# Optimization experiments

Measured on AMD Instinct MI355X. Metric: run time of the kernel, lower is better.

## Reference

```python
import jax, jax.numpy as jnp
import numpy as np

R = 3           # disp_range = (3, 3)
DU = 2 * R + 1  # 7 displacements per axis, 49 total
PNAMES = ['mn_w1','mn_b1','mn_w2','mn_b2','mn_w3','mn_b3','mn_w4','mn_b4','mn_wd','mn_bd','mn_w5','mn_b5','dap_w','dap_b','me_w1','me_b1','me_w2','me_b2','me_w3','me_b3','gz1_w','gz1_b','gr1_w','gr1_b','gq1_w','gq1_b','gz2_w','gz2_b','gr2_w','gr2_b','gq2_w','gq2_b','fh_w1','fh_b1','fh_w2','fh_b2']


def conv2d(x, w, b, stride=(1, 1), padding=((1, 1), (1, 1))):
    y = jax.lax.conv_general_dilated(x, w, stride, padding, dimension_numbers=('NCHW', 'OIHW', 'NCHW'))
    return y + b[None, :, None, None]


def warp_backwards(f, flow):
    # bilinear backward warp with zero padding; flow[:,0]=u (x offset), flow[:,1]=v (y offset)
    B, C, H, W = f.shape
    gy, gx = jnp.meshgrid(jnp.arange(H, dtype=flow.dtype), jnp.arange(W, dtype=flow.dtype), indexing='ij')
    x = gx[None] + flow[:, 0]
    y = gy[None] + flow[:, 1]
    x0, y0 = jnp.floor(x), jnp.floor(y)
    wx, wy = x - x0, y - y0

    def corner(yy, xx, wgt):
        valid = (yy >= 0) & (yy <= H - 1) & (xx >= 0) & (xx <= W - 1)
        yc = jnp.clip(yy, 0, H - 1).astype(jnp.int32)
        xc = jnp.clip(xx, 0, W - 1).astype(jnp.int32)
        g = jax.vmap(lambda fb, yb, xb: fb[:, yb, xb])(f, yc, xc)  # (B,C,H,W)
        return g * (wgt * valid.astype(f.dtype))[:, None]

    return (corner(y0, x0, (1 - wy) * (1 - wx)) + corner(y0, x0 + 1, (1 - wy) * wx)
            + corner(y0 + 1, x0, wy * (1 - wx)) + corner(y0 + 1, x0 + 1, wy * wx))


def gru_step(h, x, wz, bz, wr, br, wq, bq, pad):
    hx = jnp.concatenate([h, x], axis=1)
    z = jax.nn.sigmoid(conv2d(hx, wz, bz, padding=pad))
    r = jax.nn.sigmoid(conv2d(hx, wr, br, padding=pad))
    q = jnp.tanh(conv2d(jnp.concatenate([r * h, x], axis=1), wq, bq, padding=pad))
    return (1.0 - z) * h + z * q


def _run(fmap1, fmap2, h, flow, P):
    B, C, H, W = fmap1.shape
    lrelu, relu = jax.nn.leaky_relu, jax.nn.relu
    # backward warp of fmap2 by current (detached) flow
    f2w = warp_backwards(fmap2, jax.lax.stop_gradient(flow))
    # --- correlation volume: 49 zero-padded shifts of warped fmap2, paired with fmap1 ---
    pad2 = jnp.pad(f2w, ((0, 0), (0, 0), (R, R), (R, R)))
    # k = i*DU + j  <->  shift (di, dj) = (i-R, j-R); shifted[...,y,x] = f2w[y+dj, x+di]
    shifted = jnp.stack([pad2[:, :, j:j + H, i:i + W] for i in range(DU) for j in range(DU)], axis=1)  # (B,49,C,H,W)
    valid = (jnp.sum(shifted, axis=2, keepdims=True) != 0).astype(fmap1.dtype)
    mvol = jnp.concatenate([jnp.broadcast_to(fmap1[:, None], shifted.shape), shifted], axis=2) * valid  # (B,49,2C,H,W)
    # --- matching net, applied per displacement ---
    x = mvol.reshape(B * DU * DU, 2 * C, H, W)
    x = relu(conv2d(x, P['mn_w1'], P['mn_b1']))
    x = relu(conv2d(x, P['mn_w2'], P['mn_b2'], stride=(2, 2)))
    x = relu(conv2d(x, P['mn_w3'], P['mn_b3']))
    x = relu(conv2d(x, P['mn_w4'], P['mn_b4']))
    # ConvTranspose2d(k=4, s=2, p=1) == lhs-dilated conv with pad 2
    x = jax.lax.conv_general_dilated(x, P['mn_wd'], (1, 1), ((2, 2), (2, 2)), lhs_dilation=(2, 2), dimension_numbers=('NCHW', 'OIHW', 'NCHW')) + P['mn_bd'][None, :, None, None]
    x = relu(x)
    x = conv2d(x, P['mn_w5'], P['mn_b5'])  # (B*49, 1, H, W)
    cvol = x.reshape(B, DU * DU, H, W)
    # --- displacement-aware projection: 1x1 conv across the 49 displacement channels ---
    cvol = jnp.einsum('ok,bkhw->bohw', P['dap_w'], cvol) + P['dap_b'][None, :, None, None]
    # --- motion encoder ---
    m = jnp.concatenate([cvol, fmap1, flow], axis=1)  # (B, 49+C+2, H, W)
    m = lrelu(conv2d(m, P['me_w1'], P['me_b1']))
    m = lrelu(conv2d(m, P['me_w2'], P['me_b2']))
    m = conv2d(m, P['me_w3'], P['me_b3'])             # (B, 94, H, W)
    xg = jnp.concatenate([m, flow], axis=1)           # (B, 96, H, W)
    # --- separable conv GRU: horizontal (1x5) then vertical (5x1) pass ---
    h = gru_step(h, xg, P['gz1_w'], P['gz1_b'], P['gr1_w'], P['gr1_b'], P['gq1_w'], P['gq1_b'], ((0, 0), (2, 2)))
    h = gru_step(h, xg, P['gz2_w'], P['gz2_b'], P['gr2_w'], P['gr2_b'], P['gq2_w'], P['gq2_b'], ((2, 2), (0, 0)))
    # --- flow head: softmax over 49 displacements, expectation of displacement grid ---
    s = lrelu(jnp.einsum('oi,bihw->bohw', P['fh_w1'], h) + P['fh_b1'][None, :, None, None])
    s = lrelu(jnp.einsum('oi,bihw->bohw', P['fh_w2'], s) + P['fh_b2'][None, :, None, None])
    prob = jax.nn.softmax(s, axis=1)  # (B, 49, H, W)
    dr = jnp.arange(-R, R + 1, dtype=fmap1.dtype)
    disp = jnp.stack([jnp.broadcast_to(dr[:, None], (DU, DU)), jnp.broadcast_to(dr[None, :], (DU, DU))], axis=0).reshape(2, DU * DU)
    d = jnp.einsum('bkhw,ck->bchw', prob, disp)
    return h, flow + d


def _params(key):
    shapes = {'mn_w1': (96, 64, 3, 3), 'mn_b1': (96,), 'mn_w2': (128, 96, 3, 3), 'mn_b2': (128,), 'mn_w3': (128, 128, 3, 3), 'mn_b3': (128,), 'mn_w4': (64, 128, 3, 3), 'mn_b4': (64,), 'mn_wd': (32, 64, 4, 4), 'mn_bd': (32,), 'mn_w5': (1, 32, 3, 3), 'mn_b5': (1,), 'dap_w': (49, 49), 'dap_b': (49,), 'me_w1': (128, 83, 3, 3), 'me_b1': (128,), 'me_w2': (128, 128, 3, 3), 'me_b2': (128,), 'me_w3': (94, 128, 3, 3), 'me_b3': (94,), 'gz1_w': (128, 224, 1, 5), 'gz1_b': (128,), 'gr1_w': (128, 224, 1, 5), 'gr1_b': (128,), 'gq1_w': (128, 224, 1, 5), 'gq1_b': (128,), 'gz2_w': (128, 224, 5, 1), 'gz2_b': (128,), 'gr2_w': (128, 224, 5, 1), 'gr2_b': (128,), 'gq2_w': (128, 224, 5, 1), 'gq2_b': (128,), 'fh_w1': (256, 128), 'fh_b1': (256,), 'fh_w2': (49, 256), 'fh_b2': (49,)}
    keys = jax.random.split(key, len(shapes))
    return {n: jax.random.normal(k, s, dtype=jnp.float32) * 0.05 for (n, s), k in zip(shapes.items(), keys)}


def setup_inputs():
    key = jax.random.key(0)
    k1, k2, k3, k4, kp = jax.random.split(key, 5)
    B, C, H, W, HID = 2, 32, 64, 96, 128
    inp = {'fmap1': jax.random.normal(k1, (B, C, H, W), jnp.float32),
           'fmap2': jax.random.normal(k2, (B, C, H, W), jnp.float32),
           'h': jax.random.normal(k3, (B, HID, H, W), jnp.float32),
           'flow': jax.random.normal(k4, (B, 2, H, W), jnp.float32),
           'i': 0}
    inp.update(_params(kp))
    return inp


def reference(fmap1, fmap2, h, flow, mn_w1, mn_b1, mn_w2, mn_b2, mn_w3, mn_b3, mn_w4, mn_b4, mn_wd, mn_bd, mn_w5, mn_b5, dap_w, dap_b, me_w1, me_b1, me_w2, me_b2, me_w3, me_b3, gz1_w, gz1_b, gr1_w, gr1_b, gq1_w, gq1_b, gz2_w, gz2_b, gr2_w, gr2_b, gq2_w, gq2_b, fh_w1, fh_b1, fh_w2, fh_b2, i):
    ps = (mn_w1, mn_b1, mn_w2, mn_b2, mn_w3, mn_b3, mn_w4, mn_b4, mn_wd, mn_bd, mn_w5, mn_b5, dap_w, dap_b, me_w1, me_b1, me_w2, me_b2, me_w3, me_b3, gz1_w, gz1_b, gr1_w, gr1_b, gq1_w, gq1_b, gz2_w, gz2_b, gr2_w, gr2_b, gq2_w, gq2_b, fh_w1, fh_b1, fh_w2, fh_b2)
    return _run(fmap1, fmap2, h, flow, dict(zip(PNAMES, ps)))
```

## Files before the change

kernel.cpp:

```cpp
#include <hip/hip_runtime.h>
#include <math.h>

typedef unsigned short u16;
typedef unsigned int u32;
typedef __attribute__((ext_vector_type(8))) short bf16x8;
typedef __attribute__((ext_vector_type(4))) float f32x4;

#define HWW 6144

__device__ __forceinline__ float sigmoidf_(float x) { return 1.f / (1.f + expf(-x)); }
__device__ __forceinline__ float lrelu_(float x) { return x >= 0.f ? x : 0.01f * x; }
__device__ __forceinline__ u16 f2bf(float f) {
    u32 u = __float_as_uint(f);
    u += 0x7fffu + ((u >> 16) & 1u);
    return (u16)(u >> 16);
}
__device__ __forceinline__ float bf2f(u16 h) { return __uint_as_float(((u32)h) << 16); }
__device__ __forceinline__ u32 pk2(float a, float b) { return (u32)f2bf(a) | ((u32)f2bf(b) << 16); }

__device__ __forceinline__ void gload_lds16(const u16* g, u16* l) {
    __builtin_amdgcn_global_load_lds((const __attribute__((address_space(1))) void*)g,
                                     (__attribute__((address_space(3))) void*)l, 16, 0, 0);
}

struct WJob { const float* src; unsigned long dstOff; int OC, rowOff, IC, ICP, NT; unsigned long cum; };
struct WJobs { WJob j[16]; long total; };

__global__ __launch_bounds__(256) void k_wt_all(WJobs J, u16* __restrict__ base)
{
    long i = (long)blockIdx.x * 256 + threadIdx.x;
    if (i >= J.total) return;
    int jb = 0;
    #pragma unroll
    for (int k = 1; k < 16; ++k) if (i >= (long)J.j[k].cum) jb = k;
    WJob w = J.j[jb];
    long local = i - (long)w.cum;
    int c = (int)(local % w.ICP);
    int t = (int)((local / w.ICP) % w.NT);
    int o = (int)(local / ((long)w.ICP * w.NT));
    float val = (c < w.IC) ? w.src[((long)o * w.IC + c) * w.NT + t] : 0.f;
    base[w.dstOff + ((long)(w.rowOff + o) * w.NT + t) * w.ICP + c] = f2bf(val);
}

__global__ __launch_bounds__(256) void k_wt_dq(const float* __restrict__ w, u16* __restrict__ dst)
{
    int i = blockIdx.x * 256 + threadIdx.x;
    if (i >= 32768) return;
    int c = i & 63; int t = (i >> 6) & 3; int o = (i >> 8) & 31; int q = i >> 13;
    int ry = q >> 1, rx = q & 1, ta = t >> 1, tb = t & 1;
    int ky = ry + 2 * ta, kx = rx + 2 * tb;
    float val = w[(((long)o * 64 + c) * 4 + ky) * 4 + kx];
    dst[(long)q * 8192 + o * 256 + t * 64 + c] = f2bf(val);
}

__global__ __launch_bounds__(256) void k_wt5(const float* __restrict__ w, float* __restrict__ wt)
{
    int i = blockIdx.x * 256 + threadIdx.x;
    if (i >= 288) return;
    int t = i % 9, c = i / 9;
    wt[t * 32 + c] = w[c * 9 + t];
}

__global__ void k_catb(const float* __restrict__ a, const float* __restrict__ b, float* __restrict__ d)
{
    int i = threadIdx.x;
    if (i < 128) d[i] = a[i];
    else if (i < 256) d[i] = b[i - 128];
}

__global__ __launch_bounds__(256) void k_prep_f1(const float* __restrict__ fmap1, u16* __restrict__ f1bf)
{
    int gid = blockIdx.x * 256 + threadIdx.x;
    if (gid >= 24576) return;
    int idx = gid >> 1, half = gid & 1;
    int b = idx / HWW, p = idx % HWW;
    const float* fb = fmap1 + (long)b * 32 * HWW + p + (long)(half * 16) * HWW;
    u32 pk[8];
    #pragma unroll
    for (int c2 = 0; c2 < 8; ++c2)
        pk[c2] = pk2(fb[(long)(2 * c2) * HWW], fb[(long)(2 * c2 + 1) * HWW]);
    u16* op = f1bf + ((long)idx << 5) + half * 16;
    ((uint4*)op)[0] = make_uint4(pk[0], pk[1], pk[2], pk[3]);
    ((uint4*)op)[1] = make_uint4(pk[4], pk[5], pk[6], pk[7]);
}

__global__ __launch_bounds__(256) void k_warp(const float* __restrict__ fmap2, const float* __restrict__ flow,
                                              u16* __restrict__ f2wbf, float* __restrict__ cs)
{
    int gid = blockIdx.x * 256 + threadIdx.x;
    if (gid >= 24576) return;
    int idx = gid >> 1, half = gid & 1;
    int b = idx / HWW, p = idx % HWW, y = p / 96, x = p % 96;
    float u = flow[(b * 2 + 0) * HWW + p], v = flow[(b * 2 + 1) * HWW + p];
    float fx = (float)x + u, fy = (float)y + v;
    float fx0 = floorf(fx), fy0 = floorf(fy);
    float wx = fx - fx0, wy = fy - fy0;
    int x0 = (int)fx0, y0i = (int)fy0, x1 = x0 + 1, y1 = y0i + 1;
    bool vx0 = x0 >= 0 && x0 < 96, vx1 = x1 >= 0 && x1 < 96;
    bool vy0 = y0i >= 0 && y0i < 64, vy1 = y1 >= 0 && y1 < 64;
    float m00 = (vy0 && vx0) ? (1.f - wy) * (1.f - wx) : 0.f;
    float m01 = (vy0 && vx1) ? (1.f - wy) * wx : 0.f;
    float m10 = (vy1 && vx0) ? wy * (1.f - wx) : 0.f;
    float m11 = (vy1 && vx1) ? wy * wx : 0.f;
    int cx0 = min(max(x0, 0), 95), cx1 = min(max(x1, 0), 95);
    int cy0 = min(max(y0i, 0), 63), cy1 = min(max(y1, 0), 63);
    int i00 = cy0 * 96 + cx0, i01 = cy0 * 96 + cx1, i10 = cy1 * 96 + cx0, i11 = cy1 * 96 + cx1;
    const float* fb = fmap2 + (long)b * 32 * HWW + (long)(half * 16) * HWW;
    float s = 0.f; u32 pk[8];
    #pragma unroll
    for (int c2 = 0; c2 < 8; ++c2) {
        const float* fa = fb + (long)(2 * c2) * HWW;
        const float* fc = fb + (long)(2 * c2 + 1) * HWW;
        float g0 = m00 * fa[i00] + m01 * fa[i01] + m10 * fa[i10] + m11 * fa[i11];
        float g1 = m00 * fc[i00] + m01 * fc[i01] + m10 * fc[i10] + m11 * fc[i11];
        s += g0 + g1;
        pk[c2] = pk2(g0, g1);
    }
    u16* op = f2wbf + ((long)idx << 5) + half * 16;
    ((uint4*)op)[0] = make_uint4(pk[0], pk[1], pk[2], pk[3]);
    ((uint4*)op)[1] = make_uint4(pk[4], pk[5], pk[6], pk[7]);
    float stot = s + __shfl_xor(s, 1);
    if (half == 0) cs[idx] = stot;
}

template<int BM, int BN, int MODE, int KH, int KW, int PH, int PW, int STRIDE, int ACT, int OUTF32,
         int IH, int IW, int OH, int OW, int ICP, int NKT>
__global__ __launch_bounds__(256) void k_gemm(
    const u16* __restrict__ A0, const u16* __restrict__ A1,
    const float* __restrict__ csm, const u16* __restrict__ Wb,
    const float* __restrict__ bias, const u16* __restrict__ zpg,
    u16* __restrict__ outb, u16* __restrict__ outb2, float* __restrict__ outf,
    int OC, int ldc, int coff, int nOff)
{
    constexpr int WAVES_M = (BM == 64) ? 2 : ((BN == 128) ? 2 : 4);
    constexpr int WAVES_N = 4 / WAVES_M;
    constexpr int WTM = BM / WAVES_M;
    constexpr int WTN = BN / WAVES_N;
    constexpr int MF = WTM / 16;
    constexpr int NF = WTN / 16;
    __shared__ u16 As[2][BM * 32];
    __shared__ u16 Bs[2][BN * 32];
    int tid = threadIdx.x, lane = tid & 63, wid = tid >> 6;
    constexpr int AIW = BM / 64;
    constexpr int BI  = BN / 16;
    constexpr int BIW = (BI >= 4) ? (BI / 4) : 1;
    int ryz = 0, rxz = 0;
    if (MODE == 2) { ryz = blockIdx.z >> 1; rxz = blockIdx.z & 1; }
    const u16* WbZ = Wb + (MODE == 2 ? (long)blockIdx.z * 32 * 256 : 0);
    int n0 = blockIdx.y * BN;
    int chunk = lane & 3, sub = lane >> 2;

    const u16* aB0[AIW]; const u16* aB1[AIW]; u32 am[AIW];
    #pragma unroll
    for (int j = 0; j < AIW; ++j) {
        int row = wid * (BM / 4) + j * 16 + sub;
        int gm = blockIdx.x * BM + row;
        constexpr int OHW = (MODE == 1) ? 6144 : ((MODE == 2) ? 1536 : OH * OW);
        constexpr int OWW = (MODE == 1) ? 96 : ((MODE == 2) ? 48 : OW);
        int nI = gm / OHW, rem = gm - nI * OHW;
        int y0 = rem / OWW, x0 = rem - y0 * OWW;
        aB1[j] = A0; am[j] = 0;
        if (MODE == 0) {
            aB0[j] = A0 + ((long)nI * IH * IW + (long)y0 * STRIDE * IW + (long)x0 * STRIDE) * ICP + chunk * 8;
            u32 m = 0;
            #pragma unroll
            for (int t = 0; t < KH * KW; ++t) {
                int dy = t / KW - PH, dx = t % KW - PW;
                int iy = y0 * STRIDE + dy, ix = x0 * STRIDE + dx;
                m |= ((iy >= 0 && iy < IH && ix >= 0 && ix < IW) ? 1u : 0u) << t;
            }
            am[j] = m;
        } else if (MODE == 1) {
            int n = nOff + nI, bI = n / 49, kd = n - bI * 49;
            int di = kd / 7 - 3, dj = kd % 7 - 3;
            long bH = (long)bI * 6144;
            aB0[j] = A0 + ((bH + rem) << 5) + chunk * 8;
            aB1[j] = A1 + ((bH + (y0 + dj) * 96 + (x0 + di)) << 5) + chunk * 8;
            u32 m = 0;
            #pragma unroll
            for (int t = 0; t < 9; ++t) {
                int dy = t / 3 - 1, dx = t % 3 - 1;
                int yy = y0 + dy, xx = x0 + dx, ys = yy + dj, xs = xx + di;
                bool v = yy >= 0 && yy < 64 && xx >= 0 && xx < 96 && ys >= 0 && ys < 64 && xs >= 0 && xs < 96;
                if (v) v = (csm[bI * 6144 + ys * 96 + xs] != 0.f);
                m |= (v ? 1u : 0u) << t;
            }
            am[j] = m;
        } else {
            int iy0 = y0 + ryz - 1, ix0 = x0 + rxz - 1;
            aB0[j] = A0 + ((long)nI * 1536 + (long)iy0 * 48 + ix0) * 64 + chunk * 8;
            u32 m = 0;
            #pragma unroll
            for (int t = 0; t < 4; ++t) {
                int ta = t >> 1, tb = t & 1;
                int iy = iy0 + ta, ix = ix0 + tb;
                m |= ((iy >= 0 && iy < 32 && ix >= 0 && ix < 48) ? 1u : 0u) << t;
            }
            am[j] = m;
        }
    }
    const u16* bB[BIW];
    bool doB = (BI >= 4) || (wid < BI);
    #pragma unroll
    for (int j = 0; j < BIW; ++j) {
        int rowB = ((BI >= 4) ? wid * (BN / 4) + j * 16 : wid * 16) + sub;
        bB[j] = WbZ + (long)(n0 + rowB) * (NKT * 32) + chunk * 8;
    }

    auto stage = [&](int kt, int bn) {
        #pragma unroll
        for (int j = 0; j < AIW; ++j) {
            const u16* g;
            if (MODE == 0) {
                constexpr int KTC = ICP / 32;
                int t = kt / KTC, c0 = (kt - t * KTC) << 5;
                int dy = t / KW - PH, dx = t % KW - PW;
                bool v = (am[j] >> t) & 1u;
                g = v ? aB0[j] + (long)(dy * IW + dx) * ICP + c0 : zpg;
            } else if (MODE == 1) {
                int t = kt >> 1, half = kt & 1;
                int dy = t / 3 - 1, dx = t % 3 - 1;
                bool v = (am[j] >> t) & 1u;
                const u16* b = half ? aB1[j] : aB0[j];
                g = v ? b + ((dy * 96 + dx) << 5) : zpg;
            } else {
                int t = kt >> 1, c0 = (kt & 1) << 5;
                int ta = t >> 1, tb = t & 1;
                bool v = (am[j] >> t) & 1u;
                g = v ? aB0[j] + (ta * 48 + tb) * 64 + c0 : zpg;
            }
            gload_lds16(g, &As[bn][(wid * (BM / 4) + j * 16) * 32]);
        }
        if (doB) {
            #pragma unroll
            for (int j = 0; j < BIW; ++j) {
                int base = (BI >= 4) ? wid * (BN / 4) + j * 16 : wid * 16;
                gload_lds16(bB[j] + kt * 32, &Bs[bn][base * 32]);
            }
        }
    };

    int wm = (WAVES_N == 2) ? (wid >> 1) : wid;
    int wn = (WAVES_N == 2) ? (wid & 1) : 0;
    int fr = lane & 15, fg = lane >> 4;
    f32x4 acc[MF][NF];
    #pragma unroll
    for (int i = 0; i < MF; ++i)
        #pragma unroll
        for (int j = 0; j < NF; ++j)
            acc[i][j] = (f32x4){0.f, 0.f, 0.f, 0.f};

    stage(0, 0);
    __syncthreads();

    #pragma unroll
    for (int kt = 0; kt < NKT; ++kt) {
        int cur = kt & 1;
        if (kt + 1 < NKT) stage(kt + 1, cur ^ 1);
        bf16x8 af[MF], bv[NF];
        #pragma unroll
        for (int i = 0; i < MF; ++i)
            af[i] = *(const bf16x8*)&As[cur][(wm * WTM + i * 16 + fr) * 32 + fg * 8];
        #pragma unroll
        for (int j = 0; j < NF; ++j)
            bv[j] = *(const bf16x8*)&Bs[cur][(wn * WTN + j * 16 + fr) * 32 + fg * 8];
        #pragma unroll
        for (int i = 0; i < MF; ++i)
            #pragma unroll
            for (int j = 0; j < NF; ++j)
                acc[i][j] = __builtin_amdgcn_mfma_f32_16x16x32_bf16(af[i], bv[j], acc[i][j], 0, 0, 0);
        if (kt + 1 < NKT) __syncthreads();
    }

    #pragma unroll
    for (int i = 0; i < MF; ++i) {
        #pragma unroll
        for (int j = 0; j < NF; ++j) {
            int nn = n0 + wn * WTN + j * 16 + fr;
            if (nn >= OC) continue;
            #pragma unroll
            for (int rr = 0; rr < 4; ++rr) {
                int mloc = wm * WTM + i * 16 + fg * 4 + rr;
                long gm = (long)blockIdx.x * BM + mloc;
                float v = acc[i][j][rr] + bias[nn];
                if (ACT == 1) v = fmaxf(v, 0.f);
                else if (ACT == 2) v = lrelu_(v);
                if (OUTF32) {
                    outf[gm * ldc + coff + nn] = v;
                } else if (MODE == 2) {
                    int nI = (int)(gm / 1536); int rq = (int)(gm - (long)nI * 1536);
                    int Y = rq / 48, X = rq - (rq / 48) * 48;
                    long di = (((long)nI * 64 + 2 * Y + ryz) * 96 + (2 * X + rxz)) * 32 + nn;
                    outb[di] = f2bf(v);
                } else {
                    long di = gm * ldc + coff + nn;
                    u16 hv = f2bf(v);
                    outb[di] = hv;
                    if (outb2) outb2[di] = hv;
                }
            }
        }
    }
}

__global__ __launch_bounds__(256) void k_conv5n(const u16* __restrict__ x5, const float* __restrict__ w5t,
                                                const float* __restrict__ b5, u16* __restrict__ cvolT,
                                                int N, int n0)
{
    int idx = blockIdx.x * 256 + threadIdx.x;
    if (idx >= N * HWW) return;
    int nl = idx / HWW, p = idx % HWW, y = p / 96, x = p % 96;
    float acc = b5[0];
    #pragma unroll
    for (int t = 0; t < 9; ++t) {
        int iy = y + t / 3 - 1, ix = x + t % 3 - 1;
        if (iy < 0 || iy >= 64 || ix < 0 || ix >= 96) continue;
        const u16* sp = x5 + (((long)nl * HWW + iy * 96 + ix) << 5);
        const float* wt_ = w5t + t * 32;
        #pragma unroll
        for (int c8 = 0; c8 < 4; ++c8) {
            uint4 v = *(const uint4*)(sp + c8 * 8);
            acc = fmaf(bf2f((u16)(v.x & 0xffffu)), wt_[c8 * 8 + 0], acc);
            acc = fmaf(bf2f((u16)(v.x >> 16)),     wt_[c8 * 8 + 1], acc);
            acc = fmaf(bf2f((u16)(v.y & 0xffffu)), wt_[c8 * 8 + 2], acc);
            acc = fmaf(bf2f((u16)(v.y >> 16)),     wt_[c8 * 8 + 3], acc);
            acc = fmaf(bf2f((u16)(v.z & 0xffffu)), wt_[c8 * 8 + 4], acc);
            acc = fmaf(bf2f((u16)(v.z >> 16)),     wt_[c8 * 8 + 5], acc);
            acc = fmaf(bf2f((u16)(v.w & 0xffffu)), wt_[c8 * 8 + 6], acc);
            acc = fmaf(bf2f((u16)(v.w >> 16)),     wt_[c8 * 8 + 7], acc);
        }
    }
    int n = n0 + nl;
    int b = n / 49, k = n - b * 49;
    cvolT[((long)b * HWW + p) * 64 + k] = f2bf(acc);
}

__global__ __launch_bounds__(256) void k_me_tail(const float* __restrict__ fmap1, const float* __restrict__ flow,
                                                 u16* __restrict__ mein)
{
    int gid = blockIdx.x * 256 + threadIdx.x;
    if (gid >= 73728) return;
    int j = gid / 12288, idx = gid - j * 12288;
    int b = idx / HWW, p = idx % HWW;
    int c0 = 49 + j * 8;
    u16* mp = mein + (long)idx * 96;
    #pragma unroll
    for (int q = 0; q < 8; ++q) {
        int c = c0 + q;
        if (c >= 96) break;
        float v;
        if (c < 81) v = fmap1[((long)(b * 32 + (c - 49))) * HWW + p];
        else if (c == 81) v = flow[(b * 2 + 0) * HWW + p];
        else if (c == 82) v = flow[(b * 2 + 1) * HWW + p];
        else v = 0.f;
        mp[c] = f2bf(v);
    }
}

__global__ __launch_bounds__(256) void k_set_head(const float* __restrict__ h, const float* __restrict__ flow,
                                                  float* __restrict__ hst, u16* __restrict__ hx,
                                                  u16* __restrict__ hx2)
{
    int gid = blockIdx.x * 256 + threadIdx.x;
    if (gid >= 49152) return;
    int cq = gid / 12288, idx = gid - cq * 12288;
    int b = idx / HWW, p = idx % HWW;
    int c0 = cq * 32;
    const float* hp = h + (long)b * 128 * HWW + p;
    float* hs = hst + (long)idx * 128;
    u16* hxp = hx + (long)idx * 224;
    #pragma unroll
    for (int c = c0; c < c0 + 32; c += 8) {
        float v[8];
        #pragma unroll
        for (int q = 0; q < 8; ++q) v[q] = hp[(long)(c + q) * HWW];
        *(float4*)&hs[c] = make_float4(v[0], v[1], v[2], v[3]);
        *(float4*)&hs[c + 4] = make_float4(v[4], v[5], v[6], v[7]);
        uint4 pk = make_uint4(pk2(v[0], v[1]), pk2(v[2], v[3]), pk2(v[4], v[5]), pk2(v[6], v[7]));
        *(uint4*)&hxp[c] = pk;
    }
    if (cq == 0) {
        u16 uu = f2bf(flow[(b * 2 + 0) * HWW + p]);
        u16 vv = f2bf(flow[(b * 2 + 1) * HWW + p]);
        long o = (long)idx * 224;
        hx[o + 222] = uu; hx[o + 223] = vv;
        hx2[o + 222] = uu; hx2[o + 223] = vv;
    }
}

__global__ __launch_bounds__(256) void k_post_zr(const float* __restrict__ azr, const float* __restrict__ hst,
                                                 float* __restrict__ z, u16* __restrict__ hx2)
{
    int gid = blockIdx.x * 256 + threadIdx.x;
    if (gid >= 49152) return;
    int cq = gid / 12288, idx = gid - cq * 12288;
    int c0 = cq * 32;
    const float* ap = azr + (long)idx * 256;
    const float* hs = hst + (long)idx * 128;
    float* zp = z + (long)idx * 128;
    u16* xp = hx2 + (long)idx * 224;
    #pragma unroll
    for (int c = c0; c < c0 + 32; c += 8) {
        float4 a0 = *(const float4*)&ap[c], a1 = *(const float4*)&ap[c + 4];
        float4 r0 = *(const float4*)&ap[128 + c], r1 = *(const float4*)&ap[128 + c + 4];
        float4 h0 = *(const float4*)&hs[c], h1v = *(const float4*)&hs[c + 4];
        float z0 = sigmoidf_(a0.x), z1 = sigmoidf_(a0.y), z2 = sigmoidf_(a0.z), z3 = sigmoidf_(a0.w);
        float z4 = sigmoidf_(a1.x), z5 = sigmoidf_(a1.y), z6 = sigmoidf_(a1.z), z7 = sigmoidf_(a1.w);
        *(float4*)&zp[c] = make_float4(z0, z1, z2, z3);
        *(float4*)&zp[c + 4] = make_float4(z4, z5, z6, z7);
        float rh0 = sigmoidf_(r0.x) * h0.x, rh1 = sigmoidf_(r0.y) * h0.y;
        float rh2 = sigmoidf_(r0.z) * h0.z, rh3 = sigmoidf_(r0.w) * h0.w;
        float rh4 = sigmoidf_(r1.x) * h1v.x, rh5 = sigmoidf_(r1.y) * h1v.y;
        float rh6 = sigmoidf_(r1.z) * h1v.z, rh7 = sigmoidf_(r1.w) * h1v.w;
        uint4 pk = make_uint4(pk2(rh0, rh1), pk2(rh2, rh3), pk2(rh4, rh5), pk2(rh6, rh7));
        *(uint4*)&xp[c] = pk;
    }
}

template<int FIN>
__global__ __launch_bounds__(256) void k_post_q(const float* __restrict__ aq, const float* __restrict__ z,
                                                const float* __restrict__ hst, float* __restrict__ h1f,
                                                u16* __restrict__ hxdst, float* __restrict__ outH)
{
    int gid = blockIdx.x * 256 + threadIdx.x;
    if (gid >= 49152) return;
    int cq = gid / 12288, idx = gid - cq * 12288;
    int b = idx / HWW, p = idx % HWW;
    int c0 = cq * 32;
    const float* ap = aq + (long)idx * 128;
    const float* zp = z + (long)idx * 128;
    const float* hs = hst + (long)idx * 128;
    #pragma unroll
    for (int c = c0; c < c0 + 32; c += 8) {
        float hn[8];
        #pragma unroll
        for (int q = 0; q < 8; ++q) {
            float qq = tanhf(ap[c + q]);
            float zv = zp[c + q];
            hn[q] = (1.f - zv) * hs[c + q] + zv * qq;
        }
        uint4 pk = make_uint4(pk2(hn[0], hn[1]), pk2(hn[2], hn[3]), pk2(hn[4], hn[5]), pk2(hn[6], hn[7]));
        if (FIN == 0) {
            *(float4*)&h1f[(long)idx * 128 + c] = make_float4(hn[0], hn[1], hn[2], hn[3]);
            *(float4*)&h1f[(long)idx * 128 + c + 4] = make_float4(hn[4], hn[5], hn[6], hn[7]);
            *(uint4*)&hxdst[(long)idx * 224 + c] = pk;
        } else {
            #pragma unroll
            for (int q = 0; q < 8; ++q)
                outH[((long)(b * 128 + c + q)) * HWW + p] = hn[q];
            *(uint4*)&hxdst[(long)idx * 128 + c] = pk;
        }
    }
}

__global__ __launch_bounds__(256) void k_soft(const float* __restrict__ s2, const float* __restrict__ flow,
                                              float* __restrict__ outFlow)
{
    int idx = blockIdx.x * 256 + threadIdx.x;
    if (idx >= 12288) return;
    int b = idx / HWW, p = idx % HWW;
    const float* sp = s2 + (long)idx * 64;
    float lg[49];
    #pragma unroll
    for (int k = 0; k < 48; k += 4) {
        float4 v = *(const float4*)&sp[k];
        lg[k] = v.x; lg[k + 1] = v.y; lg[k + 2] = v.z; lg[k + 3] = v.w;
    }
    lg[48] = sp[48];
    float m = -1e30f;
    #pragma unroll
    for (int k = 0; k < 49; ++k) m = fmaxf(m, lg[k]);
    float s = 0.f, a0 = 0.f, a1 = 0.f;
    #pragma unroll
    for (int k = 0; k < 49; ++k) {
        float e = expf(lg[k] - m);
        s += e;
        a0 += e * (float)(k / 7 - 3);
        a1 += e * (float)(k % 7 - 3);
    }
    float inv = 1.f / s;
    outFlow[(long)(b * 2 + 0) * HWW + p] = flow[(long)(b * 2 + 0) * HWW + p] + a0 * inv;
    outFlow[(long)(b * 2 + 1) * HWW + p] = flow[(long)(b * 2 + 1) * HWW + p] + a1 * inv;
}

extern "C" void kernel_launch(void* const* d_in, const int* in_sizes, int n_in,
                              void* d_out, int out_size, void* d_ws, size_t ws_size,
                              hipStream_t stream)
{
    const float* fmap1 = (const float*)d_in[0];
    const float* fmap2 = (const float*)d_in[1];
    const float* h     = (const float*)d_in[2];
    const float* flow  = (const float*)d_in[3];
    int pb = (in_sizes[4] == 1) ? 5 : 4;
    const float* mn_w1 = (const float*)d_in[pb + 0];
    const float* mn_b1 = (const float*)d_in[pb + 1];
    const float* mn_w2 = (const float*)d_in[pb + 2];
    const float* mn_b2 = (const float*)d_in[pb + 3];
    const float* mn_w3 = (const float*)d_in[pb + 4];
    const float* mn_b3 = (const float*)d_in[pb + 5];
    const float* mn_w4 = (const float*)d_in[pb + 6];
    const float* mn_b4 = (const float*)d_in[pb + 7];
    const float* mn_wd = (const float*)d_in[pb + 8];
    const float* mn_bd = (const float*)d_in[pb + 9];
    const float* mn_w5 = (const float*)d_in[pb + 10];
    const float* mn_b5 = (const float*)d_in[pb + 11];
    const float* dap_w = (const float*)d_in[pb + 12];
    const float* dap_b = (const float*)d_in[pb + 13];
    const float* me_w1 = (const float*)d_in[pb + 14];
    const float* me_b1 = (const float*)d_in[pb + 15];
    const float* me_w2 = (const float*)d_in[pb + 16];
    const float* me_b2 = (const float*)d_in[pb + 17];
    const float* me_w3 = (const float*)d_in[pb + 18];
    const float* me_b3 = (const float*)d_in[pb + 19];
    const float* gz1_w = (const float*)d_in[pb + 20];
    const float* gz1_b = (const float*)d_in[pb + 21];
    const float* gr1_w = (const float*)d_in[pb + 22];
    const float* gr1_b = (const float*)d_in[pb + 23];
    const float* gq1_w = (const float*)d_in[pb + 24];
    const float* gq1_b = (const float*)d_in[pb + 25];
    const float* gz2_w = (const float*)d_in[pb + 26];
    const float* gz2_b = (const float*)d_in[pb + 27];
    const float* gr2_w = (const float*)d_in[pb + 28];
    const float* gr2_b = (const float*)d_in[pb + 29];
    const float* gq2_w = (const float*)d_in[pb + 30];
    const float* gq2_b = (const float*)d_in[pb + 31];
    const float* fh_w1 = (const float*)d_in[pb + 32];
    const float* fh_b1 = (const float*)d_in[pb + 33];
    const float* fh_w2 = (const float*)d_in[pb + 34];
    const float* fh_b2 = (const float*)d_in[pb + 35];

    char* wsB = (char*)d_ws;
    size_t off = 0;
    auto alc = [&](size_t bytes) { size_t o = off; off = (off + bytes + 255) & ~(size_t)255; return o; };

    size_t o_zpg  = alc(256);
    size_t o_wc1  = alc(128 * 576 * 2);
    size_t o_wc2  = alc(128 * 864 * 2);
    size_t o_wc3  = alc((size_t)128 * 1152 * 2);
    size_t o_wc4  = alc((size_t)64 * 1152 * 2);
    size_t o_wdq  = alc(32768 * 2);
    size_t o_wme1 = alc(128 * 864 * 2);
    size_t o_wme2 = alc((size_t)128 * 1152 * 2);
    size_t o_wme3 = alc((size_t)128 * 1152 * 2);
    size_t o_wzr1 = alc((size_t)256 * 1120 * 2);
    size_t o_wq1  = alc((size_t)128 * 1120 * 2);
    size_t o_wzr2 = alc((size_t)256 * 1120 * 2);
    size_t o_wq2  = alc((size_t)128 * 1120 * 2);
    size_t o_wfh1 = alc(256 * 128 * 2);
    size_t o_wfh2 = alc(64 * 256 * 2);
    size_t o_wdapb= alc(64 * 64 * 2);
    size_t o_w5t  = alc(288 * 4);
    size_t o_bzr1 = alc(256 * 4);
    size_t o_bzr2 = alc(256 * 4);
    size_t wArenaBytes = off;

    size_t o_f1bf = alc((size_t)12288 * 32 * 2);
    size_t o_f2wb = alc((size_t)12288 * 32 * 2);
    size_t o_cs   = alc(12288 * 4);
    size_t o_cvolT= alc((size_t)12288 * 64 * 2);

    const int CH = 49;
    size_t sharedBase = off;
    size_t offA = sharedBase;
    auto alcA = [&](size_t bytes) { size_t o = offA; offA = (offA + bytes + 255) & ~(size_t)255; return o; };
    size_t o_x1 = alcA((size_t)CH * 6144 * 96 * 2);
    size_t o_x2 = alcA((size_t)98 * 1536 * 128 * 2);
    size_t o_x3 = alcA((size_t)98 * 1536 * 128 * 2);
    size_t o_x4 = alcA((size_t)98 * 1536 * 64 * 2);
    size_t o_x5 = alcA((size_t)98 * 6144 * 32 * 2);
    size_t offB2 = sharedBase;
    auto alcB = [&](size_t bytes) { size_t o = offB2; offB2 = (offB2 + bytes + 255) & ~(size_t)255; return o; };
    size_t o_mein = alcB((size_t)12288 * 96 * 2);
    size_t o_m1   = alcB((size_t)12288 * 128 * 2);
    size_t o_m2   = alcB((size_t)12288 * 128 * 2);
    size_t o_hx   = alcB((size_t)12288 * 224 * 2);
    size_t o_hx2  = alcB((size_t)12288 * 224 * 2);
    size_t o_h2bf = alcB((size_t)12288 * 128 * 2);
    size_t o_s1b  = alcB((size_t)12288 * 256 * 2);
    size_t o_hst  = alcB((size_t)12288 * 128 * 4);
    size_t o_h1f  = alcB((size_t)12288 * 128 * 4);
    size_t o_zf   = alcB((size_t)12288 * 128 * 4);
    size_t o_azr  = alcB((size_t)12288 * 256 * 4);
    size_t o_aqf  = alcB((size_t)12288 * 128 * 4);
    size_t o_s2   = alcB((size_t)12288 * 64 * 4);

    u16* wbase = (u16*)wsB;
    u16* zpg  = (u16*)(wsB + o_zpg);
    u16* wdq  = (u16*)(wsB + o_wdq);
    float* w5t = (float*)(wsB + o_w5t);
    float* bzr1 = (float*)(wsB + o_bzr1);
    float* bzr2 = (float*)(wsB + o_bzr2);
    u16* wc1  = (u16*)(wsB + o_wc1);   u16* wc2  = (u16*)(wsB + o_wc2);
    u16* wc3  = (u16*)(wsB + o_wc3);   u16* wc4  = (u16*)(wsB + o_wc4);
    u16* wme1 = (u16*)(wsB + o_wme1);  u16* wme2 = (u16*)(wsB + o_wme2);
    u16* wme3 = (u16*)(wsB + o_wme3);
    u16* wzr1 = (u16*)(wsB + o_wzr1);  u16* wq1  = (u16*)(wsB + o_wq1);
    u16* wzr2 = (u16*)(wsB + o_wzr2);  u16* wq2  = (u16*)(wsB + o_wq2);
    u16* wfh1 = (u16*)(wsB + o_wfh1);  u16* wfh2 = (u16*)(wsB + o_wfh2);
    u16* wdapb= (u16*)(wsB + o_wdapb);

    u16* f1bf = (u16*)(wsB + o_f1bf);  u16* f2wb = (u16*)(wsB + o_f2wb);
    float* cs = (float*)(wsB + o_cs);
    u16* cvolT = (u16*)(wsB + o_cvolT);
    u16* x1 = (u16*)(wsB + o_x1); u16* x2 = (u16*)(wsB + o_x2); u16* x3 = (u16*)(wsB + o_x3);
    u16* x4 = (u16*)(wsB + o_x4); u16* x5 = (u16*)(wsB + o_x5);
    u16* mein = (u16*)(wsB + o_mein);
    u16* m1 = (u16*)(wsB + o_m1); u16* m2 = (u16*)(wsB + o_m2);
    u16* hx = (u16*)(wsB + o_hx); u16* hx2 = (u16*)(wsB + o_hx2);
    u16* h2bf = (u16*)(wsB + o_h2bf);  u16* s1b = (u16*)(wsB + o_s1b);
    float* hst = (float*)(wsB + o_hst); float* h1f = (float*)(wsB + o_h1f);
    float* zf = (float*)(wsB + o_zf); float* azr = (float*)(wsB + o_azr);
    float* aqf = (float*)(wsB + o_aqf); float* s2 = (float*)(wsB + o_s2);

    float* outH = (float*)d_out;
    float* outFlow = outH + (long)2 * 128 * HWW;

    auto nb = [](long total, int bs) { return (unsigned)((total + bs - 1) / bs); };

    hipMemsetAsync(wsB, 0, wArenaBytes, stream);
    hipMemsetAsync(wsB + o_cvolT, 0, (size_t)12288 * 64 * 2, stream);

    WJobs J;
    {
        auto mk = [](const float* src, size_t dstOffBytes, int OC, int rowOff, int IC, int ICP, int NT) {
            WJob w; w.src = src; w.dstOff = dstOffBytes / 2; w.OC = OC; w.rowOff = rowOff;
            w.IC = IC; w.ICP = ICP; w.NT = NT; w.cum = 0; return w;
        };
        J.j[0]  = mk(mn_w1, o_wc1, 96, 0, 64, 64, 9);
        J.j[1]  = mk(mn_w2, o_wc2, 128, 0, 96, 96, 9);
        J.j[2]  = mk(mn_w3, o_wc3, 128, 0, 128, 128, 9);
        J.j[3]  = mk(mn_w4, o_wc4, 64, 0, 128, 128, 9);
        J.j[4]  = mk(me_w1, o_wme1, 128, 0, 83, 96, 9);
        J.j[5]  = mk(me_w2, o_wme2, 128, 0, 128, 128, 9);
        J.j[6]  = mk(me_w3, o_wme3, 94, 0, 128, 128, 9);
        J.j[7]  = mk(gz1_w, o_wzr1, 128, 0, 224, 224, 5);
        J.j[8]  = mk(gr1_w, o_wzr1, 128, 128, 224, 224, 5);
        J.j[9]  = mk(gq1_w, o_wq1, 128, 0, 224, 224, 5);
        J.j[10] = mk(gz2_w, o_wzr2, 128, 0, 224, 224, 5);
        J.j[11] = mk(gr2_w, o_wzr2, 128, 128, 224, 224, 5);
        J.j[12] = mk(gq2_w, o_wq2, 128, 0, 224, 224, 5);
        J.j[13] = mk(fh_w1, o_wfh1, 256, 0, 128, 128, 1);
        J.j[14] = mk(fh_w2, o_wfh2, 49, 0, 256, 256, 1);
        J.j[15] = mk(dap_w, o_wdapb, 49, 0, 49, 64, 1);
        long cum = 0;
        for (int k = 0; k < 16; ++k) {
            J.j[k].cum = cum;
            cum += (long)J.j[k].OC * J.j[k].NT * J.j[k].ICP;
        }
        J.total = cum;
    }
    k_wt_all<<<nb(J.total, 256), 256, 0, stream>>>(J, wbase);
    k_wt_dq<<<nb(32768, 256), 256, 0, stream>>>(mn_wd, wdq);
    k_wt5<<<2, 256, 0, stream>>>(mn_w5, w5t);
    k_catb<<<1, 256, 0, stream>>>(gz1_b, gr1_b, bzr1);
    k_catb<<<1, 256, 0, stream>>>(gz2_b, gr2_b, bzr2);

    k_prep_f1<<<nb(24576, 256), 256, 0, stream>>>(fmap1, f1bf);
    k_warp<<<nb(24576, 256), 256, 0, stream>>>(fmap2, flow, f2wb, cs);

    for (int n0 = 0; n0 < 98; n0 += CH) {
        k_gemm<128,128,1,3,3,1,1,1,1,0,64,96,64,96,32,18><<<dim3(2352, 1), 256, 0, stream>>>(
            f1bf, f2wb, cs, wc1, mn_b1, zpg, x1, nullptr, nullptr, 96, 96, 0, n0);
        k_gemm<128,128,0,3,3,1,1,2,1,0,64,96,32,48,96,27><<<dim3(588, 1), 256, 0, stream>>>(
            x1, nullptr, nullptr, wc2, mn_b2, zpg, x2 + (long)n0 * 196608, nullptr, nullptr, 128, 128, 0, 0);
    }
    k_gemm<128,128,0,3,3,1,1,1,1,0,32,48,32,48,128,36><<<dim3(1176, 1), 256, 0, stream>>>(
        x2, nullptr, nullptr, wc3, mn_b3, zpg, x3, nullptr, nullptr, 128, 128, 0, 0);
    k_gemm<128,64,0,3,3,1,1,1,1,0,32,48,32,48,128,36><<<dim3(1176, 1), 256, 0, stream>>>(
        x3, nullptr, nullptr, wc4, mn_b4, zpg, x4, nullptr, nullptr, 64, 64, 0, 0);
    k_gemm<128,32,2,4,4,2,2,1,1,0,32,48,32,48,64,8><<<dim3(1176, 1, 4), 256, 0, stream>>>(
        x4, nullptr, nullptr, wdq, mn_bd, zpg, x5, nullptr, nullptr, 32, 32, 0, 0);
    k_conv5n<<<nb(98L * HWW, 256), 256, 0, stream>>>(x5, w5t, mn_b5, cvolT, 98, 0);

    k_gemm<64,64,0,1,1,0,0,1,0,0,64,96,64,96,64,2><<<dim3(192, 1), 256, 0, stream>>>(
        cvolT, nullptr, nullptr, wdapb, dap_b, zpg, mein, nullptr, nullptr, 49, 96, 0, 0);
    k_me_tail<<<nb(73728, 256), 256, 0, stream>>>(fmap1, flow, mein);

    k_gemm<64,128,0,3,3,1,1,1,2,0,64,96,64,96,96,27><<<dim3(192, 1), 256, 0, stream>>>(
        mein, nullptr, nullptr, wme1, me_b1, zpg, m1, nullptr, nullptr, 128, 128, 0, 0);
    k_gemm<64,128,0,3,3,1,1,1,2,0,64,96,64,96,128,36><<<dim3(192, 1), 256, 0, stream>>>(
        m1, nullptr, nullptr, wme2, me_b2, zpg, m2, nullptr, nullptr, 128, 128, 0, 0);
    k_gemm<64,128,0,3,3,1,1,1,0,0,64,96,64,96,128,36><<<dim3(192, 1), 256, 0, stream>>>(
        m2, nullptr, nullptr, wme3, me_b3, zpg, hx, hx2, nullptr, 94, 224, 128, 0);

    k_set_head<<<nb(49152, 256), 256, 0, stream>>>(h, flow, hst, hx, hx2);
    k_gemm<64,128,0,1,5,0,2,1,0,1,64,96,64,96,224,35><<<dim3(192, 2), 256, 0, stream>>>(
        hx, nullptr, nullptr, wzr1, bzr1, zpg, nullptr, nullptr, azr, 256, 256, 0, 0);
    k_post_zr<<<nb(49152, 256), 256, 0, stream>>>(azr, hst, zf, hx2);
    k_gemm<64,128,0,1,5,0,2,1,0,1,64,96,64,96,224,35><<<dim3(192, 1), 256, 0, stream>>>(
        hx2, nullptr, nullptr, wq1, gq1_b, zpg, nullptr, nullptr, aqf, 128, 128, 0, 0);
    k_post_q<0><<<nb(49152, 256), 256, 0, stream>>>(aqf, zf, hst, h1f, hx, nullptr);

    k_gemm<64,128,0,5,1,2,0,1,0,1,64,96,64,96,224,35><<<dim3(192, 2), 256, 0, stream>>>(
        hx, nullptr, nullptr, wzr2, bzr2, zpg, nullptr, nullptr, azr, 256, 256, 0, 0);
    k_post_zr<<<nb(49152, 256), 256, 0, stream>>>(azr, h1f, zf, hx2);
    k_gemm<64,128,0,5,1,2,0,1,0,1,64,96,64,96,224,35><<<dim3(192, 1), 256, 0, stream>>>(
        hx2, nullptr, nullptr, wq2, gq2_b, zpg, nullptr, nullptr, aqf, 128, 128, 0, 0);
    k_post_q<1><<<nb(49152, 256), 256, 0, stream>>>(aqf, zf, h1f, nullptr, h2bf, outH);

    k_gemm<64,128,0,1,1,0,0,1,2,0,64,96,64,96,128,4><<<dim3(192, 2), 256, 0, stream>>>(
        h2bf, nullptr, nullptr, wfh1, fh_b1, zpg, s1b, nullptr, nullptr, 256, 256, 0, 0);
    k_gemm<64,64,0,1,1,0,0,1,2,1,64,96,64,96,256,8><<<dim3(192, 1), 256, 0, stream>>>(
        s1b, nullptr, nullptr, wfh2, fh_b2, zpg, nullptr, nullptr, s2, 49, 64, 0, 0);
    k_soft<<<nb(12288, 256), 256, 0, stream>>>(s2, flow, outFlow);
}
```

Baseline: 730.8 us.

## Fuse GRU gate epilogues into GEMMs and trim N-tile to 96

Moves the GRU z/r sigmoid, r*h product and q tanh/state-update epilogues into the conv GEMM output stage, so the separate post kernels and the fp32 azr/aqf intermediate buffers are gone. It also generalises the wave split and B-tile loading so BN=96 tiles work, and uses them for the first correlation conv and me3, where OC is 96 or 94, to avoid computing padded columns. The fused epilogue uses scattered scalar stores and adds extra memory reads per output element, which may be less coalesced than the dedicated vectorised kernels.

```diff
diff --git a/kernel.cpp b/kernel.cpp
--- a/kernel.cpp
+++ b/kernel.cpp
@@ -132,8 +132,8 @@
     u16* __restrict__ outb, u16* __restrict__ outb2, float* __restrict__ outf,
     int OC, int ldc, int coff, int nOff)
 {
-    constexpr int WAVES_M = (BM == 64) ? 2 : ((BN == 128) ? 2 : 4);
-    constexpr int WAVES_N = 4 / WAVES_M;
+    constexpr int WAVES_N = (BN >= 128) ? 2 : 1;
+    constexpr int WAVES_M = 4 / WAVES_N;
     constexpr int WTM = BM / WAVES_M;
     constexpr int WTN = BN / WAVES_N;
     constexpr int MF = WTM / 16;
@@ -142,8 +142,8 @@
     __shared__ u16 Bs[2][BN * 32];
     int tid = threadIdx.x, lane = tid & 63, wid = tid >> 6;
     constexpr int AIW = BM / 64;
-    constexpr int BI  = BN / 16;
-    constexpr int BIW = (BI >= 4) ? (BI / 4) : 1;
+    constexpr int BG  = BN / 16;
+    constexpr int BJW = (BG + 3) / 4;
     int ryz = 0, rxz = 0;
     if (MODE == 2) { ryz = blockIdx.z >> 1; rxz = blockIdx.z & 1; }
     const u16* WbZ = Wb + (MODE == 2 ? (long)blockIdx.z * 32 * 256 : 0);
@@ -199,12 +199,12 @@
             am[j] = m;
         }
     }
-    const u16* bB[BIW];
-    bool doB = (BI >= 4) || (wid < BI);
-    #pragma unroll
-    for (int j = 0; j < BIW; ++j) {
-        int rowB = ((BI >= 4) ? wid * (BN / 4) + j * 16 : wid * 16) + sub;
-        bB[j] = WbZ + (long)(n0 + rowB) * (NKT * 32) + chunk * 8;
+    const u16* bB[BJW];
+    #pragma unroll
+    for (int j = 0; j < BJW; ++j) {
+        int g = wid + 4 * j;
+        int gc = (g < BG) ? g : 0;
+        bB[j] = WbZ + (long)(n0 + gc * 16 + sub) * (NKT * 32) + chunk * 8;
     }
 
     auto stage = [&](int kt, int bn) {
@@ -231,12 +231,10 @@
             }
             gload_lds16(g, &As[bn][(wid * (BM / 4) + j * 16) * 32]);
         }
-        if (doB) {
-            #pragma unroll
-            for (int j = 0; j < BIW; ++j) {
-                int base = (BI >= 4) ? wid * (BN / 4) + j * 16 : wid * 16;
-                gload_lds16(bB[j] + kt * 32, &Bs[bn][base * 32]);
-            }
+        #pragma unroll
+        for (int j = 0; j < BJW; ++j) {
+            int g = wid + 4 * j;
+            if (g < BG) gload_lds16(bB[j] + kt * 32, &Bs[bn][g * 512]);
         }
     };
 
@@ -285,8 +283,23 @@
                 float v = acc[i][j][rr] + bias[nn];
                 if (ACT == 1) v = fmaxf(v, 0.f);
                 else if (ACT == 2) v = lrelu_(v);
-                if (OUTF32) {
+                if (OUTF32 == 1) {
                     outf[gm * ldc + coff + nn] = v;
+                } else if (OUTF32 == 2) {
+                    float s = sigmoidf_(v);
+                    if (nn < 128) outf[gm * 128 + nn] = s;
+                    else outb[gm * 224 + (nn - 128)] = f2bf(s * csm[gm * 128 + (nn - 128)]);
+                } else if (OUTF32 == 3 || OUTF32 == 4) {
+                    float zv = ((const float*)A1)[gm * 128 + nn];
+                    float hnew = (1.f - zv) * csm[gm * 128 + nn] + zv * tanhf(v);
+                    if (OUTF32 == 3) {
+                        outf[gm * 128 + nn] = hnew;
+                        outb[gm * 224 + nn] = f2bf(hnew);
+                    } else {
+                        int bb = (int)(gm / 6144), pp = (int)(gm - (long)bb * 6144);
+                        outf[((long)(bb * 128 + nn)) * 6144 + pp] = hnew;
+                        outb[gm * 128 + nn] = f2bf(hnew);
+                    }
                 } else if (MODE == 2) {
                     int nI = (int)(gm / 1536); int rq = (int)(gm - (long)nI * 1536);
                     int Y = rq / 48, X = rq - (rq / 48) * 48;
@@ -385,71 +398,6 @@
         long o = (long)idx * 224;
         hx[o + 222] = uu; hx[o + 223] = vv;
         hx2[o + 222] = uu; hx2[o + 223] = vv;
-    }
-}
-
-__global__ __launch_bounds__(256) void k_post_zr(const float* __restrict__ azr, const float* __restrict__ hst,
-                                                 float* __restrict__ z, u16* __restrict__ hx2)
-{
-    int gid = blockIdx.x * 256 + threadIdx.x;
-    if (gid >= 49152) return;
-    int cq = gid / 12288, idx = gid - cq * 12288;
-    int c0 = cq * 32;
-    const float* ap = azr + (long)idx * 256;
-    const float* hs = hst + (long)idx * 128;
-    float* zp = z + (long)idx * 128;
-    u16* xp = hx2 + (long)idx * 224;
-    #pragma unroll
-    for (int c = c0; c < c0 + 32; c += 8) {
-        float4 a0 = *(const float4*)&ap[c], a1 = *(const float4*)&ap[c + 4];
-        float4 r0 = *(const float4*)&ap[128 + c], r1 = *(const float4*)&ap[128 + c + 4];
-        float4 h0 = *(const float4*)&hs[c], h1v = *(const float4*)&hs[c + 4];
-        float z0 = sigmoidf_(a0.x), z1 = sigmoidf_(a0.y), z2 = sigmoidf_(a0.z), z3 = sigmoidf_(a0.w);
-        float z4 = sigmoidf_(a1.x), z5 = sigmoidf_(a1.y), z6 = sigmoidf_(a1.z), z7 = sigmoidf_(a1.w);
-        *(float4*)&zp[c] = make_float4(z0, z1, z2, z3);
-        *(float4*)&zp[c + 4] = make_float4(z4, z5, z6, z7);
-        float rh0 = sigmoidf_(r0.x) * h0.x, rh1 = sigmoidf_(r0.y) * h0.y;
-        float rh2 = sigmoidf_(r0.z) * h0.z, rh3 = sigmoidf_(r0.w) * h0.w;
-        float rh4 = sigmoidf_(r1.x) * h1v.x, rh5 = sigmoidf_(r1.y) * h1v.y;
-        float rh6 = sigmoidf_(r1.z) * h1v.z, rh7 = sigmoidf_(r1.w) * h1v.w;
-        uint4 pk = make_uint4(pk2(rh0, rh1), pk2(rh2, rh3), pk2(rh4, rh5), pk2(rh6, rh7));
-        *(uint4*)&xp[c] = pk;
-    }
-}
-
-template<int FIN>
-__global__ __launch_bounds__(256) void k_post_q(const float* __restrict__ aq, const float* __restrict__ z,
-                                                const float* __restrict__ hst, float* __restrict__ h1f,
-                                                u16* __restrict__ hxdst, float* __restrict__ outH)
-{
-    int gid = blockIdx.x * 256 + threadIdx.x;
-    if (gid >= 49152) return;
-    int cq = gid / 12288, idx = gid - cq * 12288;
-    int b = idx / HWW, p = idx % HWW;
-    int c0 = cq * 32;
-    const float* ap = aq + (long)idx * 128;
-    const float* zp = z + (long)idx * 128;
-    const float* hs = hst + (long)idx * 128;
-    #pragma unroll
-    for (int c = c0; c < c0 + 32; c += 8) {
-        float hn[8];
-        #pragma unroll
-        for (int q = 0; q < 8; ++q) {
-            float qq = tanhf(ap[c + q]);
-            float zv = zp[c + q];
-            hn[q] = (1.f - zv) * hs[c + q] + zv * qq;
-        }
-        uint4 pk = make_uint4(pk2(hn[0], hn[1]), pk2(hn[2], hn[3]), pk2(hn[4], hn[5]), pk2(hn[6], hn[7]));
-        if (FIN == 0) {
-            *(float4*)&h1f[(long)idx * 128 + c] = make_float4(hn[0], hn[1], hn[2], hn[3]);
-            *(float4*)&h1f[(long)idx * 128 + c + 4] = make_float4(hn[4], hn[5], hn[6], hn[7]);
-            *(uint4*)&hxdst[(long)idx * 224 + c] = pk;
-        } else {
-            #pragma unroll
-            for (int q = 0; q < 8; ++q)
-                outH[((long)(b * 128 + c + q)) * HWW + p] = hn[q];
-            *(uint4*)&hxdst[(long)idx * 128 + c] = pk;
-        }
     }
 }
 
@@ -580,8 +528,6 @@
     size_t o_hst  = alcB((size_t)12288 * 128 * 4);
     size_t o_h1f  = alcB((size_t)12288 * 128 * 4);
     size_t o_zf   = alcB((size_t)12288 * 128 * 4);
-    size_t o_azr  = alcB((size_t)12288 * 256 * 4);
-    size_t o_aqf  = alcB((size_t)12288 * 128 * 4);
     size_t o_s2   = alcB((size_t)12288 * 64 * 4);
 
     u16* wbase = (u16*)wsB;
@@ -609,8 +555,8 @@
     u16* hx = (u16*)(wsB + o_hx); u16* hx2 = (u16*)(wsB + o_hx2);
     u16* h2bf = (u16*)(wsB + o_h2bf);  u16* s1b = (u16*)(wsB + o_s1b);
     float* hst = (float*)(wsB + o_hst); float* h1f = (float*)(wsB + o_h1f);
-    float* zf = (float*)(wsB + o_zf); float* azr = (float*)(wsB + o_azr);
-    float* aqf = (float*)(wsB + o_aqf); float* s2 = (float*)(wsB + o_s2);
+    float* zf = (float*)(wsB + o_zf);
+    float* s2 = (float*)(wsB + o_s2);
 
     float* outH = (float*)d_out;
     float* outFlow = outH + (long)2 * 128 * HWW;
@@ -659,7 +605,7 @@
     k_warp<<<nb(24576, 256), 256, 0, stream>>>(fmap2, flow, f2wb, cs);
 
     for (int n0 = 0; n0 < 98; n0 += CH) {
-        k_gemm<128,128,1,3,3,1,1,1,1,0,64,96,64,96,32,18><<<dim3(2352, 1), 256, 0, stream>>>(
+        k_gemm<128,96,1,3,3,1,1,1,1,0,64,96,64,96,32,18><<<dim3(2352, 1), 256, 0, stream>>>(
             f1bf, f2wb, cs, wc1, mn_b1, zpg, x1, nullptr, nullptr, 96, 96, 0, n0);
         k_gemm<128,128,0,3,3,1,1,2,1,0,64,96,32,48,96,27><<<dim3(588, 1), 256, 0, stream>>>(
             x1, nullptr, nullptr, wc2, mn_b2, zpg, x2 + (long)n0 * 196608, nullptr, nullptr, 128, 128, 0, 0);
@@ -680,23 +626,19 @@
         mein, nullptr, nullptr, wme1, me_b1, zpg, m1, nullptr, nullptr, 128, 128, 0, 0);
     k_gemm<64,128,0,3,3,1,1,1,2,0,64,96,64,96,128,36><<<dim3(192, 1), 256, 0, stream>>>(
         m1, nullptr, nullptr, wme2, me_b2, zpg, m2, nullptr, nullptr, 128, 128, 0, 0);
-    k_gemm<64,128,0,3,3,1,1,1,0,0,64,96,64,96,128,36><<<dim3(192, 1), 256, 0, stream>>>(
+    k_gemm<64,96,0,3,3,1,1,1,0,0,64,96,64,96,128,36><<<dim3(192, 1), 256, 0, stream>>>(
         m2, nullptr, nullptr, wme3, me_b3, zpg, hx, hx2, nullptr, 94, 224, 128, 0);
 
     k_set_head<<<nb(49152, 256), 256, 0, stream>>>(h, flow, hst, hx, hx2);
-    k_gemm<64,128,0,1,5,0,2,1,0,1,64,96,64,96,224,35><<<dim3(192, 2), 256, 0, stream>>>(
-        hx, nullptr, nullptr, wzr1, bzr1, zpg, nullptr, nullptr, azr, 256, 256, 0, 0);
-    k_post_zr<<<nb(49152, 256), 256, 0, stream>>>(azr, hst, zf, hx2);
-    k_gemm<64,128,0,1,5,0,2,1,0,1,64,96,64,96,224,35><<<dim3(192, 1), 256, 0, stream>>>(
-        hx2, nullptr, nullptr, wq1, gq1_b, zpg, nullptr, nullptr, aqf, 128, 128, 0, 0);
-    k_post_q<0><<<nb(49152, 256), 256, 0, stream>>>(aqf, zf, hst, h1f, hx, nullptr);
-
-    k_gemm<64,128,0,5,1,2,0,1,0,1,64,96,64,96,224,35><<<dim3(192, 2), 256, 0, stream>>>(
-        hx, nullptr, nullptr, wzr2, bzr2, zpg, nullptr, nullptr, azr, 256, 256, 0, 0);
-    k_post_zr<<<nb(49152, 256), 256, 0, stream>>>(azr, h1f, zf, hx2);
-    k_gemm<64,128,0,5,1,2,0,1,0,1,64,96,64,96,224,35><<<dim3(192, 1), 256, 0, stream>>>(
-        hx2, nullptr, nullptr, wq2, gq2_b, zpg, nullptr, nullptr, aqf, 128, 128, 0, 0);
-    k_post_q<1><<<nb(49152, 256), 256, 0, stream>>>(aqf, zf, h1f, nullptr, h2bf, outH);
+    k_gemm<64,128,0,1,5,0,2,1,0,2,64,96,64,96,224,35><<<dim3(192, 2), 256, 0, stream>>>(
+        hx, nullptr, hst, wzr1, bzr1, zpg, hx2, nullptr, zf, 256, 256, 0, 0);
+    k_gemm<64,128,0,1,5,0,2,1,0,3,64,96,64,96,224,35><<<dim3(192, 1), 256, 0, stream>>>(
+        hx2, (const u16*)zf, hst, wq1, gq1_b, zpg, hx, nullptr, h1f, 128, 128, 0, 0);
+
+    k_gemm<64,128,0,5,1,2,0,1,0,2,64,96,64,96,224,35><<<dim3(192, 2), 256, 0, stream>>>(
+        hx, nullptr, h1f, wzr2, bzr2, zpg, hx2, nullptr, zf, 256, 256, 0, 0);
+    k_gemm<64,128,0,5,1,2,0,1,0,4,64,96,64,96,224,35><<<dim3(192, 1), 256, 0, stream>>>(
+        hx2, (const u16*)zf, h1f, wq2, gq2_b, zpg, h2bf, nullptr, outH, 128, 128, 0, 0);
 
     k_gemm<64,128,0,1,1,0,0,1,2,0,64,96,64,96,128,4><<<dim3(192, 2), 256, 0, stream>>>(
         h2bf, nullptr, nullptr, wfh1, fh_b1, zpg, s1b, nullptr, nullptr, 256, 256, 0, 0);
```

Measured after the change: 669.1 us. 8.4% less time.
